# Optimization experiments

Hardware: AMD Instinct MI355X
Metric: run time of the kernel (lower is better)

Reference implementation:

```python
import jax, jax.numpy as jnp
import numpy as np

N_NODES = 40000
N_EDGES = 640000
D = 128  # in_channels == out_channels (required by the module's math)


def setup_inputs() -> dict:
    key = jax.random.key(0)
    ks = jax.random.split(key, 8)
    s = 1.0 / np.sqrt(D)  # torch Linear default init scale
    x = jax.random.normal(ks[0], (N_NODES, D), dtype=jnp.float32)
    edge_index = jax.random.randint(ks[1], (2, N_EDGES), 0, N_NODES, dtype=jnp.int64)
    Wn_w = jax.random.uniform(ks[2], (D, D), jnp.float32, -s, s)
    Wn_b = jax.random.uniform(ks[3], (D,), jnp.float32, -s, s)
    Wg_w = jax.random.uniform(ks[4], (D, D), jnp.float32, -s, s)
    Wg_b = jax.random.uniform(ks[5], (D,), jnp.float32, -s, s)
    Wa_w = jax.random.uniform(ks[6], (D, D), jnp.float32, -s, s)
    Wa_b = jax.random.uniform(ks[7], (D,), jnp.float32, -s, s)
    return {"x": x, "edge_index": edge_index,
            "Wn_w": Wn_w, "Wn_b": Wn_b,
            "Wg_w": Wg_w, "Wg_b": Wg_b,
            "Wa_w": Wa_w, "Wa_b": Wa_b}


def reference(x, edge_index, Wn_w, Wn_b, Wg_w, Wg_b, Wa_w, Wa_b):
    row, col = edge_index[0], edge_index[1]
    x_col = x[col]                                  # [E, D] gather
    alpha = jax.nn.sigmoid(x_col @ Wa_w + Wa_b)     # [E, D] edge attention
    neigh = x_col * alpha                           # [E, D]
    aggr = jax.ops.segment_sum(neigh, row, num_segments=x.shape[0])  # [N, D]
    out = jnp.tanh((x @ Wn_w + Wn_b) + (aggr @ Wg_w + Wg_b))
    return out  # dropout p=0.0 is identity
```

## Files before the change

### kernel.cpp

```cpp
#include <hip/hip_runtime.h>

#define NN 40000
#define NE 640000
#define D 128
#define CAP 64

typedef __attribute__((ext_vector_type(8))) short short8;
typedef __attribute__((ext_vector_type(4))) float f32x4;
typedef __attribute__((ext_vector_type(4))) int i32x4;

__device__ __forceinline__ short f2b(float v) {
  unsigned int u = __builtin_bit_cast(unsigned int, v);
  u = (u + 0x7fffu + ((u >> 16) & 1u)) >> 16;
  return (short)u;
}
__device__ __forceinline__ float b2f(short s) {
  unsigned int u = ((unsigned int)(unsigned short)s) << 16;
  return __builtin_bit_cast(float, u);
}

__global__ __launch_bounds__(256) void k_prep(
    const float* __restrict__ Wn, const float* __restrict__ Wg,
    const float* __restrict__ Wa, short* __restrict__ WnT,
    short* __restrict__ WgThi, short* __restrict__ WgTlo,
    short* __restrict__ WaT, int* __restrict__ cnt, short* __restrict__ h) {
  int i = blockIdx.x * 256 + threadIdx.x;
  int k = i >> 7, c = i & 127;
  WnT[c * D + k] = f2b(Wn[k * D + c]);
  WaT[c * D + k] = f2b(Wa[k * D + c]);
  float v = Wg[k * D + c];
  short hi = f2b(v);
  WgThi[c * D + k] = hi;
  WgTlo[c * D + k] = f2b(v - b2f(hi));
  if (i < 10000) {
    i32x4 z = {0, 0, 0, 0};
    *(i32x4*)(cnt + i * 4) = z;
  }
  if (i < 16) {
    short8 z = {0, 0, 0, 0, 0, 0, 0, 0};
    *(short8*)(h + (size_t)NN * D + i * 8) = z;
  }
}

__global__ __launch_bounds__(256) void k_fill(
    const int* __restrict__ ei, int* __restrict__ cnt,
    unsigned short* __restrict__ bucket) {
  int e = blockIdx.x * 256 + threadIdx.x;
  if (e >= NE) return;
  int r = ei[e];
  int c = ei[NE + e];
  int slot = atomicAdd(&cnt[r], 1);
  if (slot < CAP) bucket[(size_t)r * CAP + slot] = (unsigned short)c;
}

__global__ __launch_bounds__(256) void k_node(
    const float* __restrict__ x, const short* __restrict__ WaT,
    const float* __restrict__ ba, short* __restrict__ h_out) {
  __shared__ float xs[16][132];
  __shared__ float al_s[16][132];
  int r0 = blockIdx.x * 16;
  int t = threadIdx.x;
  int w = t >> 6, l = t & 63;
  int g = l >> 4, c16 = l & 15;

#pragma unroll
  for (int p = 0; p < 2; ++p) {
    int idx = t + p * 256;
    int row = idx >> 5, cv = idx & 31;
    f32x4 v = *(const f32x4*)(x + (size_t)(r0 + row) * D + cv * 4);
    *(f32x4*)&xs[row][cv * 4] = v;
  }
  __syncthreads();

  short8 a[4];
#pragma unroll
  for (int kt = 0; kt < 4; ++kt) {
    f32x4 v0 = *(const f32x4*)&xs[c16][kt * 32 + g * 8];
    f32x4 v1 = *(const f32x4*)&xs[c16][kt * 32 + g * 8 + 4];
    short8 tt;
    tt[0] = f2b(v0[0]); tt[1] = f2b(v0[1]); tt[2] = f2b(v0[2]); tt[3] = f2b(v0[3]);
    tt[4] = f2b(v1[0]); tt[5] = f2b(v1[1]); tt[6] = f2b(v1[2]); tt[7] = f2b(v1[3]);
    a[kt] = tt;
  }

#pragma unroll
  for (int u = 0; u < 2; ++u) {
    int ct = w * 2 + u;
    int cc = ct * 16 + c16;
    f32x4 c = {0.f, 0.f, 0.f, 0.f};
#pragma unroll
    for (int kt = 0; kt < 4; ++kt) {
      short8 b = *(const short8*)(WaT + (size_t)cc * D + kt * 32 + g * 8);
      c = __builtin_amdgcn_mfma_f32_16x16x32_bf16(a[kt], b, c, 0, 0, 0);
    }
    float bav = ba[cc];
#pragma unroll
    for (int r = 0; r < 4; ++r) {
      float tv = c[r] + bav;
      al_s[g * 4 + r][cc] = 1.0f / (1.0f + __expf(-tv));
    }
  }
  __syncthreads();

  short8 hh;
#pragma unroll
  for (int q = 0; q < 8; ++q) {
    float av = al_s[c16][w * 32 + g * 8 + q];
    float xv = xs[c16][w * 32 + g * 8 + q];
    hh[q] = f2b(xv * av);
  }
  *(short8*)(h_out + (size_t)(r0 + c16) * D + w * 32 + g * 8) = hh;
}

#define SSTEP(S0, CA, CB, CC, CD)                                   \
  {                                                                 \
    int q0 = (S0) + g < deg ? (CA) : NN;                            \
    int q1 = (S0) + 4 + g < deg ? (CB) : NN;                        \
    int q2 = (S0) + 8 + g < deg ? (CC) : NN;                        \
    int q3 = (S0) + 12 + g < deg ? (CD) : NN;                       \
    short8 v0 = *(const short8*)(h + (size_t)q0 * D + i * 8);       \
    short8 v1 = *(const short8*)(h + (size_t)q1 * D + i * 8);       \
    short8 v2 = *(const short8*)(h + (size_t)q2 * D + i * 8);       \
    short8 v3 = *(const short8*)(h + (size_t)q3 * D + i * 8);       \
    _Pragma("unroll") for (int q = 0; q < 8; ++q) {                 \
      acc[q] += b2f(v0[q]) + b2f(v1[q]);                            \
      acc[q] += b2f(v2[q]) + b2f(v3[q]);                            \
    }                                                               \
  }

__global__ __launch_bounds__(256) void k_aggr(
    const int* __restrict__ cnt, const unsigned short* __restrict__ bucket,
    const short* __restrict__ h, float* __restrict__ s) {
  int l = threadIdx.x & 63;
  int n = blockIdx.x * 4 + (threadIdx.x >> 6);
  if (n >= NN) return;
  int g = l >> 4, i = l & 15;
  int deg = cnt[n];
  deg = deg < CAP ? deg : CAP;
  int bc = bucket[(size_t)n * CAP + l];
  float acc[8];
#pragma unroll
  for (int q = 0; q < 8; ++q) acc[q] = 0.f;

  int c0 = __shfl(bc, g), c1 = __shfl(bc, 4 + g);
  int c2 = __shfl(bc, 8 + g), c3 = __shfl(bc, 12 + g);
  SSTEP(0, c0, c1, c2, c3);
  if (deg > 16) {
    int c4 = __shfl(bc, 16 + g), c5 = __shfl(bc, 20 + g);
    int c6 = __shfl(bc, 24 + g), c7 = __shfl(bc, 28 + g);
    SSTEP(16, c4, c5, c6, c7);
  }
  if (deg > 32) {
    for (int j = 32; j < deg; j += 16) {
      int d0 = __shfl(bc, (j + g) & 63), d1 = __shfl(bc, (j + 4 + g) & 63);
      int d2 = __shfl(bc, (j + 8 + g) & 63), d3 = __shfl(bc, (j + 12 + g) & 63);
      SSTEP(j, d0, d1, d2, d3);
    }
  }

#pragma unroll
  for (int q = 0; q < 8; ++q) {
    acc[q] += __shfl_xor(acc[q], 16);
    acc[q] += __shfl_xor(acc[q], 32);
  }
  if (g == 0) {
    f32x4 lo = {acc[0], acc[1], acc[2], acc[3]};
    f32x4 hi = {acc[4], acc[5], acc[6], acc[7]};
    *(f32x4*)(s + (size_t)n * D + i * 8) = lo;
    *(f32x4*)(s + (size_t)n * D + i * 8 + 4) = hi;
  }
}

__global__ __launch_bounds__(256) void k_final(
    const float* __restrict__ x, const float* __restrict__ s,
    const short* __restrict__ WnT, const short* __restrict__ WgThi,
    const short* __restrict__ WgTlo, const float* __restrict__ bn,
    const float* __restrict__ bg, float* __restrict__ out) {
  __shared__ float xs[16][132];
  __shared__ float ss[16][132];
  int r0 = blockIdx.x * 16;
  int t = threadIdx.x;
  int w = t >> 6, l = t & 63;
  int g = l >> 4, c16 = l & 15;

#pragma unroll
  for (int p = 0; p < 2; ++p) {
    int idx = t + p * 256;
    int row = idx >> 5, cv = idx & 31;
    *(f32x4*)&xs[row][cv * 4] =
        *(const f32x4*)(x + (size_t)(r0 + row) * D + cv * 4);
    *(f32x4*)&ss[row][cv * 4] =
        *(const f32x4*)(s + (size_t)(r0 + row) * D + cv * 4);
  }
  __syncthreads();

  short8 axf[4], sh[4], sl[4];
#pragma unroll
  for (int kt = 0; kt < 4; ++kt) {
    f32x4 xv0 = *(const f32x4*)&xs[c16][kt * 32 + g * 8];
    f32x4 xv1 = *(const f32x4*)&xs[c16][kt * 32 + g * 8 + 4];
    short8 tx;
    tx[0] = f2b(xv0[0]); tx[1] = f2b(xv0[1]); tx[2] = f2b(xv0[2]); tx[3] = f2b(xv0[3]);
    tx[4] = f2b(xv1[0]); tx[5] = f2b(xv1[1]); tx[6] = f2b(xv1[2]); tx[7] = f2b(xv1[3]);
    axf[kt] = tx;
    f32x4 sv0 = *(const f32x4*)&ss[c16][kt * 32 + g * 8];
    f32x4 sv1 = *(const f32x4*)&ss[c16][kt * 32 + g * 8 + 4];
    short8 th, tl;
#pragma unroll
    for (int jq = 0; jq < 4; ++jq) {
      short hh = f2b(sv0[jq]);
      th[jq] = hh;
      tl[jq] = f2b(sv0[jq] - b2f(hh));
    }
#pragma unroll
    for (int jq = 0; jq < 4; ++jq) {
      short hh = f2b(sv1[jq]);
      th[4 + jq] = hh;
      tl[4 + jq] = f2b(sv1[jq] - b2f(hh));
    }
    sh[kt] = th;
    sl[kt] = tl;
  }

#pragma unroll
  for (int u = 0; u < 2; ++u) {
    int ct = w * 2 + u;
    int cc = ct * 16 + c16;
    f32x4 c = {0.f, 0.f, 0.f, 0.f};
#pragma unroll
    for (int kt = 0; kt < 4; ++kt) {
      short8 bwn = *(const short8*)(WnT + (size_t)cc * D + kt * 32 + g * 8);
      short8 bh = *(const short8*)(WgThi + (size_t)cc * D + kt * 32 + g * 8);
      short8 bl = *(const short8*)(WgTlo + (size_t)cc * D + kt * 32 + g * 8);
      c = __builtin_amdgcn_mfma_f32_16x16x32_bf16(axf[kt], bwn, c, 0, 0, 0);
      c = __builtin_amdgcn_mfma_f32_16x16x32_bf16(sh[kt], bh, c, 0, 0, 0);
      c = __builtin_amdgcn_mfma_f32_16x16x32_bf16(sl[kt], bh, c, 0, 0, 0);
      c = __builtin_amdgcn_mfma_f32_16x16x32_bf16(sh[kt], bl, c, 0, 0, 0);
    }
    float bias = bn[cc] + bg[cc];
#pragma unroll
    for (int r = 0; r < 4; ++r) {
      int rr = r0 + g * 4 + r;
      out[(size_t)rr * D + cc] = tanhf(c[r] + bias);
    }
  }
}

extern "C" void kernel_launch(void* const* d_in, const int* in_sizes, int n_in,
                              void* d_out, int out_size, void* d_ws,
                              size_t ws_size, hipStream_t stream) {
  const float* x = (const float*)d_in[0];
  const int* ei = (const int*)d_in[1];
  const float* Wn_w = (const float*)d_in[2];
  const float* Wn_b = (const float*)d_in[3];
  const float* Wg_w = (const float*)d_in[4];
  const float* Wg_b = (const float*)d_in[5];
  const float* Wa_w = (const float*)d_in[6];
  const float* Wa_b = (const float*)d_in[7];

  char* ws = (char*)d_ws;
  short* WaT = (short*)(ws + 0);
  short* WnT = (short*)(ws + 32 * 1024);
  short* WgThi = (short*)(ws + 64 * 1024);
  short* WgTlo = (short*)(ws + 96 * 1024);
  int* cnt = (int*)(ws + 128 * 1024);
  size_t off = 512 * 1024;
  short* h = (short*)(ws + off);
  off += (size_t)(NN + 1) * D * 2;
  unsigned short* bucket = (unsigned short*)(ws + off);
  off += (size_t)NN * CAP * 2;
  float* s = (float*)(ws + off);
  float* out = (float*)d_out;

  k_prep<<<64, 256, 0, stream>>>(Wn_w, Wg_w, Wa_w, WnT, WgThi, WgTlo, WaT,
                                 cnt, h);
  k_fill<<<(NE + 255) / 256, 256, 0, stream>>>(ei, cnt, bucket);
  k_node<<<NN / 16, 256, 0, stream>>>(x, WaT, Wa_b, h);
  k_aggr<<<NN / 4, 256, 0, stream>>>(cnt, bucket, h, s);
  k_final<<<NN / 16, 256, 0, stream>>>(x, s, WnT, WgThi, WgTlo, Wn_b, Wg_b,
                                       out);
}
```

Baseline: 111.3 us.

## Apply Wg before aggregation and fuse final tanh into aggregation kernel

Uses linearity to move the Wg projection ahead of the segment sum: the node kernel now computes per-node h@Wg (fp32) and x@Wn (written into out), and the aggregation kernel sums projected rows, adds x@Wn plus the bias sum, and applies tanh. This removes the separate final GEMM kernel and the s intermediate round trip. In exchange the gathered rows are now fp32 instead of bf16, which doubles gather traffic in the aggregation. The precision of h also changes: it is rounded to bf16 before the split Wg multiply, while before the fp32 sum was split into hi and lo parts.

Measured after the change: 127.6 us. +14.7%, slower.

```diff
diff --git a/kernel.cpp b/kernel.cpp
--- a/kernel.cpp
+++ b/kernel.cpp
@@ -21,9 +21,11 @@
 
 __global__ __launch_bounds__(256) void k_prep(
     const float* __restrict__ Wn, const float* __restrict__ Wg,
-    const float* __restrict__ Wa, short* __restrict__ WnT,
+    const float* __restrict__ Wa, const float* __restrict__ bn,
+    const float* __restrict__ bg, short* __restrict__ WnT,
     short* __restrict__ WgThi, short* __restrict__ WgTlo,
-    short* __restrict__ WaT, int* __restrict__ cnt, short* __restrict__ h) {
+    short* __restrict__ WaT, int* __restrict__ cnt, float* __restrict__ hg,
+    float* __restrict__ bsum) {
   int i = blockIdx.x * 256 + threadIdx.x;
   int k = i >> 7, c = i & 127;
   WnT[c * D + k] = f2b(Wn[k * D + c]);
@@ -36,10 +38,11 @@
     i32x4 z = {0, 0, 0, 0};
     *(i32x4*)(cnt + i * 4) = z;
   }
-  if (i < 16) {
-    short8 z = {0, 0, 0, 0, 0, 0, 0, 0};
-    *(short8*)(h + (size_t)NN * D + i * 8) = z;
-  }
+  if (i < 32) {
+    f32x4 z = {0.f, 0.f, 0.f, 0.f};
+    *(f32x4*)(hg + (size_t)NN * D + i * 4) = z;
+  }
+  if (i < 128) bsum[i] = bn[i] + bg[i];
 }
 
 __global__ __launch_bounds__(256) void k_fill(
@@ -55,7 +58,9 @@
 
 __global__ __launch_bounds__(256) void k_node(
     const float* __restrict__ x, const short* __restrict__ WaT,
-    const float* __restrict__ ba, short* __restrict__ h_out) {
+    const short* __restrict__ WnT, const short* __restrict__ WgThi,
+    const short* __restrict__ WgTlo, const float* __restrict__ ba,
+    float* __restrict__ hg, float* __restrict__ xn_out) {
   __shared__ float xs[16][132];
   __shared__ float al_s[16][132];
   int r0 = blockIdx.x * 16;
@@ -102,14 +107,40 @@
   }
   __syncthreads();
 
-  short8 hh;
-#pragma unroll
-  for (int q = 0; q < 8; ++q) {
-    float av = al_s[c16][w * 32 + g * 8 + q];
-    float xv = xs[c16][w * 32 + g * 8 + q];
-    hh[q] = f2b(xv * av);
-  }
-  *(short8*)(h_out + (size_t)(r0 + c16) * D + w * 32 + g * 8) = hh;
+  short8 ha[4];
+#pragma unroll
+  for (int kt = 0; kt < 4; ++kt) {
+    short8 tt;
+#pragma unroll
+    for (int q = 0; q < 8; ++q) {
+      int ch = kt * 32 + g * 8 + q;
+      tt[q] = f2b(xs[c16][ch] * al_s[c16][ch]);
+    }
+    ha[kt] = tt;
+  }
+
+#pragma unroll
+  for (int u = 0; u < 2; ++u) {
+    int ct = w * 2 + u;
+    int cc = ct * 16 + c16;
+    f32x4 cn = {0.f, 0.f, 0.f, 0.f};
+    f32x4 cg = {0.f, 0.f, 0.f, 0.f};
+#pragma unroll
+    for (int kt = 0; kt < 4; ++kt) {
+      short8 bwn = *(const short8*)(WnT + (size_t)cc * D + kt * 32 + g * 8);
+      short8 bh = *(const short8*)(WgThi + (size_t)cc * D + kt * 32 + g * 8);
+      short8 bl = *(const short8*)(WgTlo + (size_t)cc * D + kt * 32 + g * 8);
+      cn = __builtin_amdgcn_mfma_f32_16x16x32_bf16(a[kt], bwn, cn, 0, 0, 0);
+      cg = __builtin_amdgcn_mfma_f32_16x16x32_bf16(ha[kt], bh, cg, 0, 0, 0);
+      cg = __builtin_amdgcn_mfma_f32_16x16x32_bf16(ha[kt], bl, cg, 0, 0, 0);
+    }
+#pragma unroll
+    for (int r = 0; r < 4; ++r) {
+      int rr = r0 + g * 4 + r;
+      xn_out[(size_t)rr * D + cc] = cn[r];
+      hg[(size_t)rr * D + cc] = cg[r];
+    }
+  }
 }
 
 #define SSTEP(S0, CA, CB, CC, CD)                                   \
@@ -118,22 +149,26 @@
     int q1 = (S0) + 4 + g < deg ? (CB) : NN;                        \
     int q2 = (S0) + 8 + g < deg ? (CC) : NN;                        \
     int q3 = (S0) + 12 + g < deg ? (CD) : NN;                       \
-    short8 v0 = *(const short8*)(h + (size_t)q0 * D + i * 8);       \
-    short8 v1 = *(const short8*)(h + (size_t)q1 * D + i * 8);       \
-    short8 v2 = *(const short8*)(h + (size_t)q2 * D + i * 8);       \
-    short8 v3 = *(const short8*)(h + (size_t)q3 * D + i * 8);       \
-    _Pragma("unroll") for (int q = 0; q < 8; ++q) {                 \
-      acc[q] += b2f(v0[q]) + b2f(v1[q]);                            \
-      acc[q] += b2f(v2[q]) + b2f(v3[q]);                            \
+    const float* p0 = hg + (size_t)q0 * D + i * 8;                  \
+    const float* p1 = hg + (size_t)q1 * D + i * 8;                  \
+    const float* p2 = hg + (size_t)q2 * D + i * 8;                  \
+    const float* p3 = hg + (size_t)q3 * D + i * 8;                  \
+    f32x4 v0a = *(const f32x4*)p0, v0b = *(const f32x4*)(p0 + 4);   \
+    f32x4 v1a = *(const f32x4*)p1, v1b = *(const f32x4*)(p1 + 4);   \
+    f32x4 v2a = *(const f32x4*)p2, v2b = *(const f32x4*)(p2 + 4);   \
+    f32x4 v3a = *(const f32x4*)p3, v3b = *(const f32x4*)(p3 + 4);   \
+    _Pragma("unroll") for (int q = 0; q < 4; ++q) {                 \
+      acc[q] += v0a[q] + v1a[q] + v2a[q] + v3a[q];                  \
+      acc[4 + q] += v0b[q] + v1b[q] + v2b[q] + v3b[q];              \
     }                                                               \
   }
 
-__global__ __launch_bounds__(256) void k_aggr(
+__global__ __launch_bounds__(256) void k_aggf(
     const int* __restrict__ cnt, const unsigned short* __restrict__ bucket,
-    const short* __restrict__ h, float* __restrict__ s) {
+    const float* __restrict__ hg, const float* __restrict__ bsum,
+    float* __restrict__ out) {
   int l = threadIdx.x & 63;
   int n = blockIdx.x * 4 + (threadIdx.x >> 6);
-  if (n >= NN) return;
   int g = l >> 4, i = l & 15;
   int deg = cnt[n];
   deg = deg < CAP ? deg : CAP;
@@ -164,85 +199,19 @@
     acc[q] += __shfl_xor(acc[q], 32);
   }
   if (g == 0) {
-    f32x4 lo = {acc[0], acc[1], acc[2], acc[3]};
-    f32x4 hi = {acc[4], acc[5], acc[6], acc[7]};
-    *(f32x4*)(s + (size_t)n * D + i * 8) = lo;
-    *(f32x4*)(s + (size_t)n * D + i * 8 + 4) = hi;
-  }
-}
-
-__global__ __launch_bounds__(256) void k_final(
-    const float* __restrict__ x, const float* __restrict__ s,
-    const short* __restrict__ WnT, const short* __restrict__ WgThi,
-    const short* __restrict__ WgTlo, const float* __restrict__ bn,
-    const float* __restrict__ bg, float* __restrict__ out) {
-  __shared__ float xs[16][132];
-  __shared__ float ss[16][132];
-  int r0 = blockIdx.x * 16;
-  int t = threadIdx.x;
-  int w = t >> 6, l = t & 63;
-  int g = l >> 4, c16 = l & 15;
-
-#pragma unroll
-  for (int p = 0; p < 2; ++p) {
-    int idx = t + p * 256;
-    int row = idx >> 5, cv = idx & 31;
-    *(f32x4*)&xs[row][cv * 4] =
-        *(const f32x4*)(x + (size_t)(r0 + row) * D + cv * 4);
-    *(f32x4*)&ss[row][cv * 4] =
-        *(const f32x4*)(s + (size_t)(r0 + row) * D + cv * 4);
-  }
-  __syncthreads();
-
-  short8 axf[4], sh[4], sl[4];
-#pragma unroll
-  for (int kt = 0; kt < 4; ++kt) {
-    f32x4 xv0 = *(const f32x4*)&xs[c16][kt * 32 + g * 8];
-    f32x4 xv1 = *(const f32x4*)&xs[c16][kt * 32 + g * 8 + 4];
-    short8 tx;
-    tx[0] = f2b(xv0[0]); tx[1] = f2b(xv0[1]); tx[2] = f2b(xv0[2]); tx[3] = f2b(xv0[3]);
-    tx[4] = f2b(xv1[0]); tx[5] = f2b(xv1[1]); tx[6] = f2b(xv1[2]); tx[7] = f2b(xv1[3]);
-    axf[kt] = tx;
-    f32x4 sv0 = *(const f32x4*)&ss[c16][kt * 32 + g * 8];
-    f32x4 sv1 = *(const f32x4*)&ss[c16][kt * 32 + g * 8 + 4];
-    short8 th, tl;
-#pragma unroll
-    for (int jq = 0; jq < 4; ++jq) {
-      short hh = f2b(sv0[jq]);
-      th[jq] = hh;
-      tl[jq] = f2b(sv0[jq] - b2f(hh));
-    }
-#pragma unroll
-    for (int jq = 0; jq < 4; ++jq) {
-      short hh = f2b(sv1[jq]);
-      th[4 + jq] = hh;
-      tl[4 + jq] = f2b(sv1[jq] - b2f(hh));
-    }
-    sh[kt] = th;
-    sl[kt] = tl;
-  }
-
-#pragma unroll
-  for (int u = 0; u < 2; ++u) {
-    int ct = w * 2 + u;
-    int cc = ct * 16 + c16;
-    f32x4 c = {0.f, 0.f, 0.f, 0.f};
-#pragma unroll
-    for (int kt = 0; kt < 4; ++kt) {
-      short8 bwn = *(const short8*)(WnT + (size_t)cc * D + kt * 32 + g * 8);
-      short8 bh = *(const short8*)(WgThi + (size_t)cc * D + kt * 32 + g * 8);
-      short8 bl = *(const short8*)(WgTlo + (size_t)cc * D + kt * 32 + g * 8);
-      c = __builtin_amdgcn_mfma_f32_16x16x32_bf16(axf[kt], bwn, c, 0, 0, 0);
-      c = __builtin_amdgcn_mfma_f32_16x16x32_bf16(sh[kt], bh, c, 0, 0, 0);
-      c = __builtin_amdgcn_mfma_f32_16x16x32_bf16(sl[kt], bh, c, 0, 0, 0);
-      c = __builtin_amdgcn_mfma_f32_16x16x32_bf16(sh[kt], bl, c, 0, 0, 0);
-    }
-    float bias = bn[cc] + bg[cc];
-#pragma unroll
-    for (int r = 0; r < 4; ++r) {
-      int rr = r0 + g * 4 + r;
-      out[(size_t)rr * D + cc] = tanhf(c[r] + bias);
-    }
+    float* po = out + (size_t)n * D + i * 8;
+    f32x4 x0 = *(const f32x4*)po;
+    f32x4 x1 = *(const f32x4*)(po + 4);
+    f32x4 b0 = *(const f32x4*)(bsum + i * 8);
+    f32x4 b1 = *(const f32x4*)(bsum + i * 8 + 4);
+    f32x4 o0, o1;
+#pragma unroll
+    for (int q = 0; q < 4; ++q) {
+      o0[q] = tanhf(acc[q] + x0[q] + b0[q]);
+      o1[q] = tanhf(acc[4 + q] + x1[q] + b1[q]);
+    }
+    *(f32x4*)po = o0;
+    *(f32x4*)(po + 4) = o1;
   }
 }
 
@@ -263,20 +232,18 @@
   short* WnT = (short*)(ws + 32 * 1024);
   short* WgThi = (short*)(ws + 64 * 1024);
   short* WgTlo = (short*)(ws + 96 * 1024);
-  int* cnt = (int*)(ws + 128 * 1024);
+  float* bsum = (float*)(ws + 128 * 1024);
+  int* cnt = (int*)(ws + 132 * 1024);
   size_t off = 512 * 1024;
-  short* h = (short*)(ws + off);
-  off += (size_t)(NN + 1) * D * 2;
+  float* hg = (float*)(ws + off);
+  off += (size_t)(NN + 1) * D * 4;
   unsigned short* bucket = (unsigned short*)(ws + off);
-  off += (size_t)NN * CAP * 2;
-  float* s = (float*)(ws + off);
   float* out = (float*)d_out;
 
-  k_prep<<<64, 256, 0, stream>>>(Wn_w, Wg_w, Wa_w, WnT, WgThi, WgTlo, WaT,
-                                 cnt, h);
+  k_prep<<<64, 256, 0, stream>>>(Wn_w, Wg_w, Wa_w, Wn_b, Wg_b, WnT, WgThi,
+                                 WgTlo, WaT, cnt, hg, bsum);
   k_fill<<<(NE + 255) / 256, 256, 0, stream>>>(ei, cnt, bucket);
-  k_node<<<NN / 16, 256, 0, stream>>>(x, WaT, Wa_b, h);
-  k_aggr<<<NN / 4, 256, 0, stream>>>(cnt, bucket, h, s);
-  k_final<<<NN / 16, 256, 0, stream>>>(x, s, WnT, WgThi, WgTlo, Wn_b, Wg_b,
-                                       out);
-}
+  k_node<<<NN / 16, 256, 0, stream>>>(x, WaT, WnT, WgThi, WgTlo, Wa_b, hg,
+                                      out);
+  k_aggf<<<NN / 4, 256, 0, stream>>>(cnt, bucket, hg, bsum, out);
+}
```

## Precompute bf16 x and hi/lo split aggregates upstream; widen final kernel to 512 threads

Applied to the files above, without the earlier changes.

k_node now writes its bf16 conversion of x to a workspace buffer, and k_aggr emits each aggregate as a packed bf16 hi/lo pair instead of fp32. k_final reads these directly, which halves the x read and drops the per-element conversions. It now runs 8 waves per block, each handling one 16-column tile, with separate accumulators for the Wn and Wg products. The cost is an extra 10 MB xbf write in k_node and more pressure on the split kernels. The n>=NN guard was also removed, which is safe only because NN divides evenly.

Result: no change. 113.1 us (+1.6%).

```diff
diff --git a/kernel.cpp b/kernel.cpp
--- a/kernel.cpp
+++ b/kernel.cpp
@@ -55,7 +55,8 @@
 
 __global__ __launch_bounds__(256) void k_node(
     const float* __restrict__ x, const short* __restrict__ WaT,
-    const float* __restrict__ ba, short* __restrict__ h_out) {
+    const float* __restrict__ ba, short* __restrict__ h_out,
+    short* __restrict__ xbf_out) {
   __shared__ float xs[16][132];
   __shared__ float al_s[16][132];
   int r0 = blockIdx.x * 16;
@@ -81,6 +82,7 @@
     tt[0] = f2b(v0[0]); tt[1] = f2b(v0[1]); tt[2] = f2b(v0[2]); tt[3] = f2b(v0[3]);
     tt[4] = f2b(v1[0]); tt[5] = f2b(v1[1]); tt[6] = f2b(v1[2]); tt[7] = f2b(v1[3]);
     a[kt] = tt;
+    *(short8*)(xbf_out + (size_t)(r0 + c16) * D + kt * 32 + g * 8) = tt;
   }
 
 #pragma unroll
@@ -130,10 +132,9 @@
 
 __global__ __launch_bounds__(256) void k_aggr(
     const int* __restrict__ cnt, const unsigned short* __restrict__ bucket,
-    const short* __restrict__ h, float* __restrict__ s) {
+    const short* __restrict__ h, unsigned int* __restrict__ ssplit) {
   int l = threadIdx.x & 63;
   int n = blockIdx.x * 4 + (threadIdx.x >> 6);
-  if (n >= NN) return;
   int g = l >> 4, i = l & 15;
   int deg = cnt[n];
   deg = deg < CAP ? deg : CAP;
@@ -164,85 +165,73 @@
     acc[q] += __shfl_xor(acc[q], 32);
   }
   if (g == 0) {
-    f32x4 lo = {acc[0], acc[1], acc[2], acc[3]};
-    f32x4 hi = {acc[4], acc[5], acc[6], acc[7]};
-    *(f32x4*)(s + (size_t)n * D + i * 8) = lo;
-    *(f32x4*)(s + (size_t)n * D + i * 8 + 4) = hi;
-  }
-}
-
-__global__ __launch_bounds__(256) void k_final(
-    const float* __restrict__ x, const float* __restrict__ s,
+    unsigned int u[8];
+#pragma unroll
+    for (int q = 0; q < 8; ++q) {
+      short hi = f2b(acc[q]);
+      short lo = f2b(acc[q] - b2f(hi));
+      u[q] = ((unsigned int)(unsigned short)hi << 16) | (unsigned short)lo;
+    }
+    *(i32x4*)(ssplit + (size_t)n * D + i * 8) = *(i32x4*)&u[0];
+    *(i32x4*)(ssplit + (size_t)n * D + i * 8 + 4) = *(i32x4*)&u[4];
+  }
+}
+
+__global__ __launch_bounds__(512) void k_final(
+    const short* __restrict__ xbf, const unsigned int* __restrict__ ssplit,
     const short* __restrict__ WnT, const short* __restrict__ WgThi,
     const short* __restrict__ WgTlo, const float* __restrict__ bn,
     const float* __restrict__ bg, float* __restrict__ out) {
-  __shared__ float xs[16][132];
-  __shared__ float ss[16][132];
+  __shared__ unsigned int xsu[16][68];
+  __shared__ unsigned int ssu[16][132];
   int r0 = blockIdx.x * 16;
   int t = threadIdx.x;
   int w = t >> 6, l = t & 63;
   int g = l >> 4, c16 = l & 15;
 
-#pragma unroll
-  for (int p = 0; p < 2; ++p) {
-    int idx = t + p * 256;
-    int row = idx >> 5, cv = idx & 31;
-    *(f32x4*)&xs[row][cv * 4] =
-        *(const f32x4*)(x + (size_t)(r0 + row) * D + cv * 4);
-    *(f32x4*)&ss[row][cv * 4] =
-        *(const f32x4*)(s + (size_t)(r0 + row) * D + cv * 4);
+  {
+    int row = t >> 5, ch = t & 31;
+    *(i32x4*)&ssu[row][ch * 4] =
+        *(const i32x4*)(ssplit + (size_t)(r0 + row) * D + ch * 4);
+    if (t < 256) {
+      int row2 = t >> 4, ch2 = t & 15;
+      *(i32x4*)&xsu[row2][ch2 * 4] =
+          *(const i32x4*)(xbf + (size_t)(r0 + row2) * D + ch2 * 8);
+    }
   }
   __syncthreads();
 
-  short8 axf[4], sh[4], sl[4];
+  int cc = w * 16 + c16;
+  f32x4 cn = {0.f, 0.f, 0.f, 0.f};
+  f32x4 cg = {0.f, 0.f, 0.f, 0.f};
 #pragma unroll
   for (int kt = 0; kt < 4; ++kt) {
-    f32x4 xv0 = *(const f32x4*)&xs[c16][kt * 32 + g * 8];
-    f32x4 xv1 = *(const f32x4*)&xs[c16][kt * 32 + g * 8 + 4];
-    short8 tx;
-    tx[0] = f2b(xv0[0]); tx[1] = f2b(xv0[1]); tx[2] = f2b(xv0[2]); tx[3] = f2b(xv0[3]);
-    tx[4] = f2b(xv1[0]); tx[5] = f2b(xv1[1]); tx[6] = f2b(xv1[2]); tx[7] = f2b(xv1[3]);
-    axf[kt] = tx;
-    f32x4 sv0 = *(const f32x4*)&ss[c16][kt * 32 + g * 8];
-    f32x4 sv1 = *(const f32x4*)&ss[c16][kt * 32 + g * 8 + 4];
-    short8 th, tl;
-#pragma unroll
-    for (int jq = 0; jq < 4; ++jq) {
-      short hh = f2b(sv0[jq]);
-      th[jq] = hh;
-      tl[jq] = f2b(sv0[jq] - b2f(hh));
-    }
-#pragma unroll
-    for (int jq = 0; jq < 4; ++jq) {
-      short hh = f2b(sv1[jq]);
-      th[4 + jq] = hh;
-      tl[4 + jq] = f2b(sv1[jq] - b2f(hh));
-    }
-    sh[kt] = th;
-    sl[kt] = tl;
-  }
-
-#pragma unroll
-  for (int u = 0; u < 2; ++u) {
-    int ct = w * 2 + u;
-    int cc = ct * 16 + c16;
-    f32x4 c = {0.f, 0.f, 0.f, 0.f};
-#pragma unroll
-    for (int kt = 0; kt < 4; ++kt) {
-      short8 bwn = *(const short8*)(WnT + (size_t)cc * D + kt * 32 + g * 8);
-      short8 bh = *(const short8*)(WgThi + (size_t)cc * D + kt * 32 + g * 8);
-      short8 bl = *(const short8*)(WgTlo + (size_t)cc * D + kt * 32 + g * 8);
-      c = __builtin_amdgcn_mfma_f32_16x16x32_bf16(axf[kt], bwn, c, 0, 0, 0);
-      c = __builtin_amdgcn_mfma_f32_16x16x32_bf16(sh[kt], bh, c, 0, 0, 0);
-      c = __builtin_amdgcn_mfma_f32_16x16x32_bf16(sl[kt], bh, c, 0, 0, 0);
-      c = __builtin_amdgcn_mfma_f32_16x16x32_bf16(sh[kt], bl, c, 0, 0, 0);
-    }
-    float bias = bn[cc] + bg[cc];
-#pragma unroll
-    for (int r = 0; r < 4; ++r) {
-      int rr = r0 + g * 4 + r;
-      out[(size_t)rr * D + cc] = tanhf(c[r] + bias);
-    }
+    short8 axf =
+        __builtin_bit_cast(short8, *(const i32x4*)&xsu[c16][kt * 16 + g * 4]);
+    i32x4 u0 = *(const i32x4*)&ssu[c16][kt * 32 + g * 8];
+    i32x4 u1 = *(const i32x4*)&ssu[c16][kt * 32 + g * 8 + 4];
+    short8 shf, slf;
+#pragma unroll
+    for (int q = 0; q < 4; ++q) {
+      unsigned int a = (unsigned int)u0[q], b = (unsigned int)u1[q];
+      shf[q] = (short)(a >> 16);
+      slf[q] = (short)(a & 0xffffu);
+      shf[4 + q] = (short)(b >> 16);
+      slf[4 + q] = (short)(b & 0xffffu);
+    }
+    short8 bwn = *(const short8*)(WnT + (size_t)cc * D + kt * 32 + g * 8);
+    short8 bh = *(const short8*)(WgThi + (size_t)cc * D + kt * 32 + g * 8);
+    short8 bl = *(const short8*)(WgTlo + (size_t)cc * D + kt * 32 + g * 8);
+    cn = __builtin_amdgcn_mfma_f32_16x16x32_bf16(axf, bwn, cn, 0, 0, 0);
+    cg = __builtin_amdgcn_mfma_f32_16x16x32_bf16(shf, bh, cg, 0, 0, 0);
+    cg = __builtin_amdgcn_mfma_f32_16x16x32_bf16(slf, bh, cg, 0, 0, 0);
+    cg = __builtin_amdgcn_mfma_f32_16x16x32_bf16(shf, bl, cg, 0, 0, 0);
+  }
+  float bias = bn[cc] + bg[cc];
+#pragma unroll
+  for (int r = 0; r < 4; ++r) {
+    int rr = r0 + g * 4 + r;
+    out[(size_t)rr * D + cc] = tanhf(cn[r] + cg[r] + bias);
   }
 }
 
@@ -267,16 +256,18 @@
   size_t off = 512 * 1024;
   short* h = (short*)(ws + off);
   off += (size_t)(NN + 1) * D * 2;
+  short* xbf = (short*)(ws + off);
+  off += (size_t)NN * D * 2;
   unsigned short* bucket = (unsigned short*)(ws + off);
   off += (size_t)NN * CAP * 2;
-  float* s = (float*)(ws + off);
+  unsigned int* ssplit = (unsigned int*)(ws + off);
   float* out = (float*)d_out;
 
   k_prep<<<64, 256, 0, stream>>>(Wn_w, Wg_w, Wa_w, WnT, WgThi, WgTlo, WaT,
                                  cnt, h);
   k_fill<<<(NE + 255) / 256, 256, 0, stream>>>(ei, cnt, bucket);
-  k_node<<<NN / 16, 256, 0, stream>>>(x, WaT, Wa_b, h);
-  k_aggr<<<NN / 4, 256, 0, stream>>>(cnt, bucket, h, s);
-  k_final<<<NN / 16, 256, 0, stream>>>(x, s, WnT, WgThi, WgTlo, Wn_b, Wg_b,
-                                       out);
-}
+  k_node<<<NN / 16, 256, 0, stream>>>(x, WaT, Wa_b, h, xbf);
+  k_aggr<<<NN / 4, 256, 0, stream>>>(cnt, bucket, h, ssplit);
+  k_final<<<NN / 16, 512, 0, stream>>>(xbf, ssplit, WnT, WgThi, WgTlo, Wn_b,
+                                       Wg_b, out);
+}
```
